# Kernel tuning notes

Measured on AMD Instinct MI355X. Metric: run time of the kernel, lower is better.

Reference implementation:

```python
import jax, jax.numpy as jnp
import numpy as np

N, S, EMB, H = 4, 2048, 512, 8
D = EMB // H  # 64


def setup_inputs() -> dict:
    key = jax.random.key(0)
    ks = jax.random.split(key, 10)
    sc = 0.02
    return {
        "x": jax.random.normal(ks[0], (N, S, EMB), dtype=jnp.float32),
        "Wq": jax.random.normal(ks[1], (D, D), dtype=jnp.float32) * sc,
        "bq": jax.random.normal(ks[2], (D,), dtype=jnp.float32) * sc,
        "Wk": jax.random.normal(ks[3], (D, D), dtype=jnp.float32) * sc,
        "bk": jax.random.normal(ks[4], (D,), dtype=jnp.float32) * sc,
        "Wv": jax.random.normal(ks[5], (D, D), dtype=jnp.float32) * sc,
        "bv": jax.random.normal(ks[6], (D,), dtype=jnp.float32) * sc,
        "E": jax.random.normal(ks[7], (1, S, D), dtype=jnp.float32),
        "Wo": jax.random.normal(ks[8], (EMB, EMB), dtype=jnp.float32) * sc,
        "bo": jax.random.normal(ks[9], (EMB,), dtype=jnp.float32) * sc,
    }


def reference(x, Wq, bq, Wk, bk, Wv, bv, E, Wo, bo):
    n, s, emb = x.shape
    h, d = H, D
    xh = x.reshape(n, s, h, d)
    # per-head Linear projections (torch Linear: y = x @ W.T + b)
    q = xh @ Wq.T + bq  # [n,s,h,d]
    k = xh @ Wk.T + bk
    v = xh @ Wv.T + bv

    # QE = queries.transpose(1,2) @ E.transpose(1,2) -> [n,h,s,s]
    QE = jnp.einsum('nqhd,sd->nhqs', q, E[0])
    # _mask_positions: zero where triu(ones(S,S),1) flipped along columns == 1
    triu1 = jnp.triu(jnp.ones((s, s), dtype=bool), 1)
    QE = jnp.where(triu1[:, ::-1], 0.0, QE)
    # _skew: pad last dim on the left, reinterpret (s, s+1) as (s+1, s), drop first row
    padded = jnp.pad(QE, ((0, 0), (0, 0), (0, 0), (1, 0)))  # [n,h,s,s+1]
    Smat = padded.reshape(n, h, s + 1, s)[:, :, 1:, :]  # [n,h,s,s]

    qk = jnp.einsum('nqhd,nkhd->nhqk', q, k)
    # faithful to source: fill where mask==0 (lower triangle incl. diag) with -1e20
    qk = jnp.where(triu1, qk, jnp.float32(-1e20))
    attention = jax.nn.softmax(qk / (emb ** 0.5), axis=3) + Smat

    z = jnp.einsum('nhql,nlhd->nqhd', attention, v).reshape(n, s, h * d)
    return z @ Wo.T + bo


if __name__ == "__main__":
    out = reference(**setup_inputs())
    print(out.shape, out.dtype)
```

## Files before the change

kernel.cpp:

```cpp
#include <hip/hip_runtime.h>
#include <hip/hip_bf16.h>

#define S_LEN 2048
#define EMB   512
#define NH    8
#define DH    64
#define NB    4

typedef float f32x4  __attribute__((ext_vector_type(4)));
typedef short short8 __attribute__((ext_vector_type(8)));

__device__ __forceinline__ unsigned short f2bf_rn(float f) {
    return __builtin_bit_cast(unsigned short, __float2bfloat16(f));
}

__device__ __forceinline__ f32x4 mfma16(short8 a, short8 b, f32x4 c) {
    return __builtin_amdgcn_mfma_f32_16x16x32_bf16(a, b, c, 0, 0, 0);
}

__device__ __forceinline__ short8 frag_read(const unsigned short* lds, int row, int oct)
{
    const char* src = (const char*)lds + row * 128 + ((oct * 16) ^ ((row & 7) << 4));
    return *reinterpret_cast<const short8*>(src);
}

__device__ __forceinline__ int pinv(int k) {
    return (k & 32) + ((k >> 2) & 3) * 8 + (k & 3) + ((k & 16) >> 2);
}

__device__ __forceinline__ void stage_tile_bf16(const unsigned short* __restrict__ g,
                                                int gstride, unsigned short* lds, int tid)
{
    #pragma unroll
    for (int c = tid; c < 512; c += 256) {
        const int r = c >> 3, s = c & 7;
        short8 v = *reinterpret_cast<const short8*>(g + (size_t)r * gstride + s * 8);
        char* dst = (char*)lds + r * 128 + ((s * 16) ^ ((r & 7) << 4));
        *reinterpret_cast<short8*>(dst) = v;
    }
}

__device__ __forceinline__ void softmax_pack(const f32x4 C[4], bool diag, int ws, int og,
                                             int rowg, float& dsum, short8& pa0, short8& pa1)
{
    constexpr float SM_SC2 = 0.06375861597263857f;
    float rs[4];
    unsigned short pw[16];
    if (!diag) {
        #pragma unroll
        for (int t = 0; t < 4; ++t) {
            float a = 0.f;
            #pragma unroll
            for (int r = 0; r < 4; ++r) {
                const float wv = __builtin_exp2f(C[t][r] * SM_SC2);
                a += wv;
                pw[t * 4 + r] = f2bf_rn(wv);
            }
            rs[t] = a;
        }
    } else {
        #pragma unroll
        for (int t = 0; t < 4; ++t) {
            float a = 0.f;
            #pragma unroll
            for (int r = 0; r < 4; ++r) {
                const bool keep = (t > ws) || (t == ws && (og * 4 + r) > rowg);
                const float wv = keep ? __builtin_exp2f(C[t][r] * SM_SC2) : 0.f;
                a += wv;
                pw[t * 4 + r] = f2bf_rn(wv);
            }
            rs[t] = a;
        }
    }
    dsum += (rs[0] + rs[1]) + (rs[2] + rs[3]);
    #pragma unroll
    for (int i = 0; i < 8; ++i) { pa0[i] = (short)pw[i]; pa1[i] = (short)pw[8 + i]; }
}

__global__ __launch_bounds__(256) void prep_w(
    const float* __restrict__ Wq, const float* __restrict__ Wk,
    const float* __restrict__ Wv, const float* __restrict__ Wo,
    unsigned short* __restrict__ wq, unsigned short* __restrict__ wk,
    unsigned short* __restrict__ wv, unsigned short* __restrict__ wo)
{
    const int i = blockIdx.x * 256 + threadIdx.x;
    if (i < 4096) {
        wq[i] = f2bf_rn(Wq[i]);
        wk[i] = f2bf_rn(Wk[i]);
        wv[i] = f2bf_rn(Wv[i]);
    }
    if (i < EMB * EMB) wo[i] = f2bf_rn(Wo[i]);
}

__global__ __launch_bounds__(256) void qkv_mfma(
    const float* __restrict__ x,
    const unsigned short* __restrict__ Wqb, const float* __restrict__ bq,
    const unsigned short* __restrict__ Wkb, const float* __restrict__ bk,
    const unsigned short* __restrict__ Wvb, const float* __restrict__ bv,
    unsigned short* __restrict__ qg, unsigned short* __restrict__ kg,
    unsigned short* __restrict__ vg)
{
    __shared__ unsigned short w_lds[3][64 * 64];

    const int tid  = threadIdx.x;
    const int lane = tid & 63;
    const int w    = tid >> 6;
    const int rowg = lane & 15;
    const int og   = lane >> 4;

    stage_tile_bf16(Wqb, 64, w_lds[0], tid);
    stage_tile_bf16(Wkb, 64, w_lds[1], tid);
    stage_tile_bf16(Wvb, 64, w_lds[2], tid);

    float bias[3][4];
    #pragma unroll
    for (int t = 0; t < 4; ++t) {
        bias[0][t] = bq[16 * t + rowg];
        bias[1][t] = bk[16 * t + rowg];
        bias[2][t] = bv[16 * t + rowg];
    }

    const int m0 = blockIdx.x * 64 + 16 * w;
    const float* xr = x + (size_t)(m0 + rowg) * 64;
    const float4 a0 = *(const float4*)(xr + og * 8);
    const float4 a1 = *(const float4*)(xr + og * 8 + 4);
    const float4 a2 = *(const float4*)(xr + 32 + og * 8);
    const float4 a3 = *(const float4*)(xr + 32 + og * 8 + 4);
    short8 af0, af1;
    af0[0] = (short)f2bf_rn(a0.x); af0[1] = (short)f2bf_rn(a0.y);
    af0[2] = (short)f2bf_rn(a0.z); af0[3] = (short)f2bf_rn(a0.w);
    af0[4] = (short)f2bf_rn(a1.x); af0[5] = (short)f2bf_rn(a1.y);
    af0[6] = (short)f2bf_rn(a1.z); af0[7] = (short)f2bf_rn(a1.w);
    af1[0] = (short)f2bf_rn(a2.x); af1[1] = (short)f2bf_rn(a2.y);
    af1[2] = (short)f2bf_rn(a2.z); af1[3] = (short)f2bf_rn(a2.w);
    af1[4] = (short)f2bf_rn(a3.x); af1[5] = (short)f2bf_rn(a3.y);
    af1[6] = (short)f2bf_rn(a3.z); af1[7] = (short)f2bf_rn(a3.w);

    __syncthreads();

    f32x4 acc[3][4];
    #pragma unroll
    for (int m = 0; m < 3; ++m)
        #pragma unroll
        for (int t = 0; t < 4; ++t) {
            const float b = bias[m][t];
            acc[m][t] = (f32x4){b, b, b, b};
        }

    #pragma unroll
    for (int m = 0; m < 3; ++m)
        #pragma unroll
        for (int t = 0; t < 4; ++t) {
            acc[m][t] = mfma16(af0, frag_read(w_lds[m], 16 * t + rowg, og),     acc[m][t]);
            acc[m][t] = mfma16(af1, frag_read(w_lds[m], 16 * t + rowg, og + 4), acc[m][t]);
        }

    unsigned short* outp[3] = {qg, kg, vg};
    #pragma unroll
    for (int m = 0; m < 3; ++m)
        #pragma unroll
        for (int r = 0; r < 4; ++r) {
            const int mr = (blockIdx.x * 64 + 16 * w) + og * 4 + r;
            const int tk = mr >> 3, h = mr & 7;
            const int n = tk >> 11, s = tk & 2047;
            const size_t rowb = (((size_t)(n * NH + h)) * S_LEN + s) * 64;
            #pragma unroll
            for (int t = 0; t < 4; ++t)
                outp[m][rowb + 16 * t + rowg] = f2bf_rn(acc[m][t][r]);
        }
}

__global__ __launch_bounds__(256) void transpose_v(
    const unsigned short* __restrict__ v, unsigned short* __restrict__ vt)
{
    __shared__ unsigned short t_lds[64][72];
    const int bid = blockIdx.x;
    const int st = bid % (S_LEN / 64);
    const int nh = bid / (S_LEN / 64);
    const unsigned short* vp = v + ((size_t)nh * S_LEN + st * 64) * DH;
    unsigned short* vtp = vt + (size_t)nh * DH * S_LEN + st * 64;
    const int tid = threadIdx.x;
    #pragma unroll
    for (int c = tid; c < 512; c += 256) {
        const int r = c >> 3, s = c & 7;
        short8 xv = *reinterpret_cast<const short8*>(vp + r * DH + s * 8);
        #pragma unroll
        for (int i = 0; i < 8; ++i) t_lds[s * 8 + i][r] = (unsigned short)xv[i];
    }
    __syncthreads();
    #pragma unroll
    for (int c = tid; c < 512; c += 256) {
        const int d = c >> 3, sc = c & 7;
        const int cb = ((sc & 4) << 3) + (sc & 3) * 4;
        short8 y;
        #pragma unroll
        for (int i = 0; i < 8; ++i)
            y[i] = (short)t_lds[d][cb + (i & 3) + ((i & 4) << 2)];
        *reinterpret_cast<short8*>(vtp + (size_t)d * S_LEN + sc * 8) = y;
    }
}

__global__ __launch_bounds__(256) void prep_e(
    const float* __restrict__ E, unsigned short* __restrict__ eb)
{
    const int i = blockIdx.x * 256 + threadIdx.x;
    if (i >= S_LEN * DH) return;
    const int dlt = i >> 6, d = i & 63;
    eb[i] = f2bf_rn(E[(size_t)(S_LEN - 1 - dlt) * DH + d]);
}

__global__ __launch_bounds__(256) void attn_mfma(
    const unsigned short* __restrict__ qg,
    const unsigned short* __restrict__ kg,
    const unsigned short* __restrict__ vtg,
    const unsigned short* __restrict__ eg,
    unsigned short* __restrict__ z)
{
    __shared__ __align__(16) unsigned short smem[20480];

    constexpr float UNI = 1.0f / 2048.0f;

    const int nqt = S_LEN / 64;
    const int bid = blockIdx.x;
    const int qt  = (nqt - 1) - (bid >> 5);
    const int nh  = bid & 31;
    const int q0  = qt * 64;
    const size_t base = (size_t)nh * S_LEN * DH;
    const unsigned short* qp = qg + base;
    const unsigned short* kp = kg + base;
    const unsigned short* vp = vtg + base;

    const int tid  = threadIdx.x;
    const int lane = tid & 63;
    const int w    = tid >> 6;
    const int rowg = lane & 15;
    const int og   = lane >> 4;

    const int r0 = tid >> 3,  s0 = tid & 7;
    const int r1 = r0 + 32;
    const int ldsoff0 = r0 * 128 + ((s0 * 16) ^ ((r0 & 7) << 4));
    const int ldsoff1 = r1 * 128 + ((s0 * 16) ^ ((r1 & 7) << 4));
    const int ksrc0 = r0 * 64 + s0 * 8,    ksrc1 = r1 * 64 + s0 * 8;
    const int vsrc0 = r0 * S_LEN + s0 * 8, vsrc1 = r1 * S_LEN + s0 * 8;

    short8 kr0, kr1, vr0, vr1;

    short8 qa0, qa1;
    {
        const unsigned short* qr = qp + (size_t)(q0 + 16 * w + rowg) * DH + og * 8;
        qa0 = *reinterpret_cast<const short8*>(qr);
        qa1 = *reinterpret_cast<const short8*>(qr + 32);
    }

    const f32x4 zero4 = {0.f, 0.f, 0.f, 0.f};
    f32x4 accS[4], accR[4];
    #pragma unroll
    for (int t = 0; t < 4; ++t) { accS[t] = zero4; accR[t] = zero4; }
    float dsum = 0.f;

    const int T = (S_LEN - q0) >> 6;
    kr0 = *(const short8*)(kp + (size_t)q0 * 64 + ksrc0);
    kr1 = *(const short8*)(kp + (size_t)q0 * 64 + ksrc1);
    vr0 = *(const short8*)(vp + q0 + vsrc0);
    vr1 = *(const short8*)(vp + q0 + vsrc1);
    *(short8*)((char*)smem + ldsoff0) = kr0;
    *(short8*)((char*)smem + ldsoff1) = kr1;
    *(short8*)((char*)(smem + 8192) + ldsoff0) = vr0;
    *(short8*)((char*)(smem + 8192) + ldsoff1) = vr1;
    __syncthreads();

    short8 pa0, pa1;
    for (int ti = 0; ti < T; ++ti) {
        const bool pf = (ti + 1 < T);
        if (pf) {
            const unsigned short* kb = kp + (size_t)(q0 + (ti + 1) * 64) * 64;
            const unsigned short* vb = vp + (q0 + (ti + 1) * 64);
            kr0 = *(const short8*)(kb + ksrc0);
            kr1 = *(const short8*)(kb + ksrc1);
            vr0 = *(const short8*)(vb + vsrc0);
            vr1 = *(const short8*)(vb + vsrc1);
        }
        const unsigned short* klds = smem + (ti & 1) * 4096;

        __builtin_amdgcn_s_setprio(1);
        f32x4 C[4];
        #pragma unroll
        for (int t = 0; t < 4; ++t) {
            const short8 kf0 = frag_read(klds, 16 * t + rowg, og);
            const short8 kf1 = frag_read(klds, 16 * t + rowg, og + 4);
            C[t] = mfma16(kf1, qa1, mfma16(kf0, qa0, zero4));
        }
        if (ti > 0) {
            const unsigned short* vprev = smem + 8192 + ((ti + 2) % 3) * 4096;
            #pragma unroll
            for (int tt = 0; tt < 4; ++tt) {
                const short8 vf0 = frag_read(vprev, 16 * tt + rowg, og);
                const short8 vf1 = frag_read(vprev, 16 * tt + rowg, og + 4);
                accS[tt] = mfma16(pa1, vf1, mfma16(pa0, vf0, accS[tt]));
            }
        }
        __builtin_amdgcn_s_setprio(0);

        if (pf) {
            unsigned short* kn = smem + ((ti + 1) & 1) * 4096;
            unsigned short* vn = smem + 8192 + ((ti + 1) % 3) * 4096;
            *(short8*)((char*)kn + ldsoff0) = kr0;
            *(short8*)((char*)kn + ldsoff1) = kr1;
            *(short8*)((char*)vn + ldsoff0) = vr0;
            *(short8*)((char*)vn + ldsoff1) = vr1;
        }
        softmax_pack(C, ti == 0, w, og, rowg, dsum, pa0, pa1);
        __syncthreads();
    }
    {
        const unsigned short* vprev = smem + 8192 + ((T + 2) % 3) * 4096;
        __builtin_amdgcn_s_setprio(1);
        #pragma unroll
        for (int tt = 0; tt < 4; ++tt) {
            const short8 vf0 = frag_read(vprev, 16 * tt + rowg, og);
            const short8 vf1 = frag_read(vprev, 16 * tt + rowg, og + 4);
            accS[tt] = mfma16(pa1, vf1, mfma16(pa0, vf0, accS[tt]));
        }
        __builtin_amdgcn_s_setprio(0);
    }
    __syncthreads();

    unsigned short* const ebuf = smem + 16384;
    const int jmax = q0 >> 6;

    kr0 = *(const short8*)(eg + ksrc0);
    kr1 = *(const short8*)(eg + ksrc1);
    vr0 = *(const short8*)(vp + q0 + vsrc0);
    vr1 = *(const short8*)(vp + q0 + vsrc1);
    {
        const short8 z8 = {0, 0, 0, 0, 0, 0, 0, 0};
        #pragma unroll
        for (int c2 = 0; c2 < 2; ++c2) {
            const int cc = lane + 64 * c2;
            const int r = 16 * w + (cc >> 3), sc = cc & 7;
            *reinterpret_cast<short8*>((char*)smem + r * 128 + sc * 16) = z8;
        }
    }
    *(short8*)((char*)ebuf + ldsoff0) = kr0;
    *(short8*)((char*)ebuf + ldsoff1) = kr1;
    *(short8*)((char*)(smem + 8192) + ldsoff0) = vr0;
    *(short8*)((char*)(smem + 8192) + ldsoff1) = vr1;
    __syncthreads();

    for (int j = 0; j <= jmax; ++j) {
        const bool pf = (j < jmax);
        if (pf) {
            const unsigned short* ebn = eg + (size_t)(j + 1) * 4096;
            const unsigned short* vbn = vp + (q0 - 64 * (j + 1));
            kr0 = *(const short8*)(ebn + ksrc0);
            kr1 = *(const short8*)(ebn + ksrc1);
            vr0 = *(const short8*)(vbn + vsrc0);
            vr1 = *(const short8*)(vbn + vsrc1);
        }
        const unsigned short* vlds = smem + 8192 + (j & 1) * 4096;

        __builtin_amdgcn_s_setprio(1);
        f32x4 G[4];
        #pragma unroll
        for (int t = 0; t < 4; ++t)
            G[t] = mfma16(qa1, frag_read(ebuf, 16 * t + rowg, og + 4),
                   mfma16(qa0, frag_read(ebuf, 16 * t + rowg, og), zero4));
        __builtin_amdgcn_s_setprio(0);

        unsigned short* pc = smem + (j & 1) * 4096;
        unsigned short* pn = smem + ((j + 1) & 1) * 4096;
        #pragma unroll
        for (int t = 0; t < 4; ++t) {
            const int c = 16 * t + rowg;
            #pragma unroll
            for (int r = 0; r < 4; ++r) {
                const int qq = 16 * w + og * 4 + r;
                float val = G[t][r];
                if (q0 + qq == S_LEN - 1) val += UNI;
                const unsigned short bv = f2bf_rn(val);
                const int swz = (qq & 7) << 4;
                if (c <= qq) {
                    const int p = pinv(qq - c);
                    *(unsigned short*)((char*)pc + qq * 128 + ((p * 2) ^ swz)) = bv;
                } else if (pf) {
                    const int p = pinv(qq - c + 64);
                    *(unsigned short*)((char*)pn + qq * 128 + ((p * 2) ^ swz)) = bv;
                }
            }
        }

        const short8 pb0 = frag_read(pc, 16 * w + rowg, og);
        const short8 pb1 = frag_read(pc, 16 * w + rowg, og + 4);
        __builtin_amdgcn_s_setprio(1);
        #pragma unroll
        for (int tt = 0; tt < 4; ++tt) {
            const short8 vf0 = frag_read(vlds, 16 * tt + rowg, og);
            const short8 vf1 = frag_read(vlds, 16 * tt + rowg, og + 4);
            accR[tt] = mfma16(pb1, vf1, mfma16(pb0, vf0, accR[tt]));
        }
        __builtin_amdgcn_s_setprio(0);

        __syncthreads();
        if (pf) {
            unsigned short* vn = smem + 8192 + ((j + 1) & 1) * 4096;
            *(short8*)((char*)ebuf + ldsoff0) = kr0;
            *(short8*)((char*)ebuf + ldsoff1) = kr1;
            *(short8*)((char*)vn + ldsoff0) = vr0;
            *(short8*)((char*)vn + ldsoff1) = vr1;
            __syncthreads();
        }
    }

    dsum += __shfl_xor(dsum, 16);
    dsum += __shfl_xor(dsum, 32);

    const int n = nh >> 3, h = nh & 7;
    const int qrow0 = q0 + 16 * w + og * 4;
    #pragma unroll
    for (int r = 0; r < 4; ++r) {
        const int qrow = qrow0 + r;
        const float dn = __shfl(dsum, og * 4 + r);
        const float inv = (qrow == S_LEN - 1) ? 0.f : 1.f / dn;
        #pragma unroll
        for (int t = 0; t < 4; ++t) {
            const float zv = accS[t][r] * inv + accR[t][r];
            z[((size_t)n * S_LEN + qrow) * EMB + h * DH + 16 * t + rowg] = f2bf_rn(zv);
        }
    }
}

__global__ __launch_bounds__(256) void outproj_mfma(
    const unsigned short* __restrict__ z,
    const unsigned short* __restrict__ Wob, const float* __restrict__ bo,
    float* __restrict__ out)
{
    __shared__ unsigned short wo_lds[2][64 * 64];

    const int tid  = threadIdx.x;
    const int lane = tid & 63;
    const int w    = tid >> 6;
    const int rowg = lane & 15;
    const int og   = lane >> 4;

    const int nob = EMB / 64;
    const int mb = blockIdx.x / nob;
    const int ob = blockIdx.x % nob;
    const int m0 = mb * 64 + 16 * w;
    const int o0 = ob * 64;

    const int r0 = tid >> 3,  s0 = tid & 7;
    const int r1 = r0 + 32;
    const int ldsoff0 = r0 * 128 + ((s0 * 16) ^ ((r0 & 7) << 4));
    const int ldsoff1 = r1 * 128 + ((s0 * 16) ^ ((r1 & 7) << 4));
    const int wsrc0 = r0 * EMB + s0 * 8, wsrc1 = r1 * EMB + s0 * 8;
    const unsigned short* wbase = Wob + (size_t)o0 * EMB;

    f32x4 acc[4];
    #pragma unroll
    for (int t = 0; t < 4; ++t) {
        const float b = bo[o0 + 16 * t + rowg];
        acc[t] = (f32x4){b, b, b, b};
    }

    short8 wr0 = *(const short8*)(wbase + wsrc0);
    short8 wr1 = *(const short8*)(wbase + wsrc1);
    *(short8*)((char*)wo_lds[0] + ldsoff0) = wr0;
    *(short8*)((char*)wo_lds[0] + ldsoff1) = wr1;
    __syncthreads();

    int cur = 0;
    for (int kt = 0; kt < 8; ++kt) {
        const bool pf = (kt < 7);
        if (pf) {
            wr0 = *(const short8*)(wbase + (kt + 1) * 64 + wsrc0);
            wr1 = *(const short8*)(wbase + (kt + 1) * 64 + wsrc1);
        }
        const unsigned short* zr = z + (size_t)(m0 + rowg) * EMB + kt * 64;
        const short8 af0 = *reinterpret_cast<const short8*>(zr + og * 8);
        const short8 af1 = *reinterpret_cast<const short8*>(zr + 32 + og * 8);
        #pragma unroll
        for (int t = 0; t < 4; ++t) {
            acc[t] = mfma16(af0, frag_read(wo_lds[cur], 16 * t + rowg, og),     acc[t]);
            acc[t] = mfma16(af1, frag_read(wo_lds[cur], 16 * t + rowg, og + 4), acc[t]);
        }
        if (pf) {
            *(short8*)((char*)wo_lds[cur ^ 1] + ldsoff0) = wr0;
            *(short8*)((char*)wo_lds[cur ^ 1] + ldsoff1) = wr1;
        }
        __syncthreads();
        cur ^= 1;
    }

    #pragma unroll
    for (int r = 0; r < 4; ++r) {
        const size_t rowb = (size_t)(m0 + og * 4 + r) * EMB + o0;
        #pragma unroll
        for (int t = 0; t < 4; ++t)
            out[rowb + 16 * t + rowg] = acc[t][r];
    }
}

extern "C" void kernel_launch(void* const* d_in, const int* in_sizes, int n_in,
                              void* d_out, int out_size, void* d_ws, size_t ws_size,
                              hipStream_t stream) {
    const float* x  = (const float*)d_in[0];
    const float* Wq = (const float*)d_in[1];
    const float* bq = (const float*)d_in[2];
    const float* Wk = (const float*)d_in[3];
    const float* bk = (const float*)d_in[4];
    const float* Wv = (const float*)d_in[5];
    const float* bv = (const float*)d_in[6];
    const float* E  = (const float*)d_in[7];
    const float* Wo = (const float*)d_in[8];
    const float* bo = (const float*)d_in[9];
    float* out = (float*)d_out;

    const size_t per = (size_t)NB * NH * S_LEN * DH;
    unsigned short* qb  = (unsigned short*)d_ws;
    unsigned short* kb  = qb  + per;
    unsigned short* vb  = kb  + per;
    unsigned short* vtb = vb  + per;
    unsigned short* eb  = vtb + per;
    unsigned short* zb  = eb + (size_t)S_LEN * DH;
    unsigned short* wqb = zb + per * 2;
    unsigned short* wkb = wqb + 4096;
    unsigned short* wvb = wkb + 4096;
    unsigned short* wob = wvb + 4096;

    prep_w<<<(EMB * EMB + 255) / 256, 256, 0, stream>>>(Wq, Wk, Wv, Wo,
                                                        wqb, wkb, wvb, wob);
    qkv_mfma<<<(NB * S_LEN * NH) / 64, 256, 0, stream>>>(x, wqb, bq, wkb, bk, wvb, bv,
                                                         qb, kb, vb);
    transpose_v<<<NB * NH * (S_LEN / 64), 256, 0, stream>>>(vb, vtb);
    prep_e<<<(S_LEN * DH + 255) / 256, 256, 0, stream>>>(E, eb);
    attn_mfma<<<NB * NH * (S_LEN / 64), 256, 0, stream>>>(qb, kb, vtb, eb, zb);
    outproj_mfma<<<(NB * S_LEN / 64) * (EMB / 64), 256, 0, stream>>>(zb, wob, bo, out);
}
```

Measured before the change: 109.4 us.

## Load E fragments directly into registers and shrink attention LDS footprint

The relative-position phase now reads E fragments straight from global memory into registers instead of staging them through an LDS buffer. This removes one LDS buffer and one barrier per iteration. The first phase's V buffer goes from triple to double buffering, which needs an extra barrier, so LDS drops from 40KB to 32KB and occupancy may rise. The separate prep_e launch is folded into the weight-conversion kernel, removing one kernel launch. The trade-off is more vector registers held for E fragments and an extra sync in the main loop.

```diff
diff --git a/kernel.cpp b/kernel.cpp
--- a/kernel.cpp
+++ b/kernel.cpp
@@ -77,11 +77,13 @@
     for (int i = 0; i < 8; ++i) { pa0[i] = (short)pw[i]; pa1[i] = (short)pw[8 + i]; }
 }
 
-__global__ __launch_bounds__(256) void prep_w(
+__global__ __launch_bounds__(256) void prep_we(
     const float* __restrict__ Wq, const float* __restrict__ Wk,
     const float* __restrict__ Wv, const float* __restrict__ Wo,
+    const float* __restrict__ E,
     unsigned short* __restrict__ wq, unsigned short* __restrict__ wk,
-    unsigned short* __restrict__ wv, unsigned short* __restrict__ wo)
+    unsigned short* __restrict__ wv, unsigned short* __restrict__ wo,
+    unsigned short* __restrict__ eb)
 {
     const int i = blockIdx.x * 256 + threadIdx.x;
     if (i < 4096) {
@@ -90,6 +92,10 @@
         wv[i] = f2bf_rn(Wv[i]);
     }
     if (i < EMB * EMB) wo[i] = f2bf_rn(Wo[i]);
+    if (i < S_LEN * DH) {
+        const int dlt = i >> 6, d = i & 63;
+        eb[i] = f2bf_rn(E[(size_t)(S_LEN - 1 - dlt) * DH + d]);
+    }
 }
 
 __global__ __launch_bounds__(256) void qkv_mfma(
@@ -200,15 +206,6 @@
     }
 }
 
-__global__ __launch_bounds__(256) void prep_e(
-    const float* __restrict__ E, unsigned short* __restrict__ eb)
-{
-    const int i = blockIdx.x * 256 + threadIdx.x;
-    if (i >= S_LEN * DH) return;
-    const int dlt = i >> 6, d = i & 63;
-    eb[i] = f2bf_rn(E[(size_t)(S_LEN - 1 - dlt) * DH + d]);
-}
-
 __global__ __launch_bounds__(256) void attn_mfma(
     const unsigned short* __restrict__ qg,
     const unsigned short* __restrict__ kg,
@@ -216,7 +213,7 @@
     const unsigned short* __restrict__ eg,
     unsigned short* __restrict__ z)
 {
-    __shared__ __align__(16) unsigned short smem[20480];
+    __shared__ __align__(16) unsigned short smem[16384];
 
     constexpr float UNI = 1.0f / 2048.0f;
 
@@ -291,7 +288,7 @@
             C[t] = mfma16(kf1, qa1, mfma16(kf0, qa0, zero4));
         }
         if (ti > 0) {
-            const unsigned short* vprev = smem + 8192 + ((ti + 2) % 3) * 4096;
+            const unsigned short* vprev = smem + 8192 + ((ti + 1) & 1) * 4096;
             #pragma unroll
             for (int tt = 0; tt < 4; ++tt) {
                 const short8 vf0 = frag_read(vprev, 16 * tt + rowg, og);
@@ -300,10 +297,11 @@
             }
         }
         __builtin_amdgcn_s_setprio(0);
+        __syncthreads();
 
         if (pf) {
             unsigned short* kn = smem + ((ti + 1) & 1) * 4096;
-            unsigned short* vn = smem + 8192 + ((ti + 1) % 3) * 4096;
+            unsigned short* vn = smem + 8192 + ((ti + 1) & 1) * 4096;
             *(short8*)((char*)kn + ldsoff0) = kr0;
             *(short8*)((char*)kn + ldsoff1) = kr1;
             *(short8*)((char*)vn + ldsoff0) = vr0;
@@ -313,7 +311,7 @@
         __syncthreads();
     }
     {
-        const unsigned short* vprev = smem + 8192 + ((T + 2) % 3) * 4096;
+        const unsigned short* vprev = smem + 8192 + ((T + 1) & 1) * 4096;
         __builtin_amdgcn_s_setprio(1);
         #pragma unroll
         for (int tt = 0; tt < 4; ++tt) {
@@ -325,13 +323,17 @@
     }
     __syncthreads();
 
-    unsigned short* const ebuf = smem + 16384;
     const int jmax = q0 >> 6;
 
-    kr0 = *(const short8*)(eg + ksrc0);
-    kr1 = *(const short8*)(eg + ksrc1);
     vr0 = *(const short8*)(vp + q0 + vsrc0);
     vr1 = *(const short8*)(vp + q0 + vsrc1);
+    short8 ef[8];
+    #pragma unroll
+    for (int t = 0; t < 4; ++t) {
+        const unsigned short* er = eg + (size_t)(16 * t + rowg) * 64;
+        ef[t * 2]     = *(const short8*)(er + og * 8);
+        ef[t * 2 + 1] = *(const short8*)(er + (og + 4) * 8);
+    }
     {
         const short8 z8 = {0, 0, 0, 0, 0, 0, 0, 0};
         #pragma unroll
@@ -341,8 +343,6 @@
             *reinterpret_cast<short8*>((char*)smem + r * 128 + sc * 16) = z8;
         }
     }
-    *(short8*)((char*)ebuf + ldsoff0) = kr0;
-    *(short8*)((char*)ebuf + ldsoff1) = kr1;
     *(short8*)((char*)(smem + 8192) + ldsoff0) = vr0;
     *(short8*)((char*)(smem + 8192) + ldsoff1) = vr1;
     __syncthreads();
@@ -350,10 +350,7 @@
     for (int j = 0; j <= jmax; ++j) {
         const bool pf = (j < jmax);
         if (pf) {
-            const unsigned short* ebn = eg + (size_t)(j + 1) * 4096;
             const unsigned short* vbn = vp + (q0 - 64 * (j + 1));
-            kr0 = *(const short8*)(ebn + ksrc0);
-            kr1 = *(const short8*)(ebn + ksrc1);
             vr0 = *(const short8*)(vbn + vsrc0);
             vr1 = *(const short8*)(vbn + vsrc1);
         }
@@ -363,9 +360,17 @@
         f32x4 G[4];
         #pragma unroll
         for (int t = 0; t < 4; ++t)
-            G[t] = mfma16(qa1, frag_read(ebuf, 16 * t + rowg, og + 4),
-                   mfma16(qa0, frag_read(ebuf, 16 * t + rowg, og), zero4));
+            G[t] = mfma16(qa1, ef[t * 2 + 1], mfma16(qa0, ef[t * 2], zero4));
         __builtin_amdgcn_s_setprio(0);
+
+        if (pf) {
+            #pragma unroll
+            for (int t = 0; t < 4; ++t) {
+                const unsigned short* er = eg + (size_t)(64 * (j + 1) + 16 * t + rowg) * 64;
+                ef[t * 2]     = *(const short8*)(er + og * 8);
+                ef[t * 2 + 1] = *(const short8*)(er + (og + 4) * 8);
+            }
+        }
 
         unsigned short* pc = smem + (j & 1) * 4096;
         unsigned short* pn = smem + ((j + 1) & 1) * 4096;
@@ -400,15 +405,12 @@
         }
         __builtin_amdgcn_s_setprio(0);
 
-        __syncthreads();
         if (pf) {
             unsigned short* vn = smem + 8192 + ((j + 1) & 1) * 4096;
-            *(short8*)((char*)ebuf + ldsoff0) = kr0;
-            *(short8*)((char*)ebuf + ldsoff1) = kr1;
             *(short8*)((char*)vn + ldsoff0) = vr0;
             *(short8*)((char*)vn + ldsoff1) = vr1;
-            __syncthreads();
-        }
+        }
+        __syncthreads();
     }
 
     dsum += __shfl_xor(dsum, 16);
@@ -527,12 +529,11 @@
     unsigned short* wvb = wkb + 4096;
     unsigned short* wob = wvb + 4096;
 
-    prep_w<<<(EMB * EMB + 255) / 256, 256, 0, stream>>>(Wq, Wk, Wv, Wo,
-                                                        wqb, wkb, wvb, wob);
+    prep_we<<<(EMB * EMB + 255) / 256, 256, 0, stream>>>(Wq, Wk, Wv, Wo, E,
+                                                         wqb, wkb, wvb, wob, eb);
     qkv_mfma<<<(NB * S_LEN * NH) / 64, 256, 0, stream>>>(x, wqb, bq, wkb, bk, wvb, bv,
                                                          qb, kb, vb);
     transpose_v<<<NB * NH * (S_LEN / 64), 256, 0, stream>>>(vb, vtb);
-    prep_e<<<(S_LEN * DH + 255) / 256, 256, 0, stream>>>(E, eb);
     attn_mfma<<<NB * NH * (S_LEN / 64), 256, 0, stream>>>(qb, kb, vtb, eb, zb);
     outproj_mfma<<<(NB * S_LEN / 64) * (EMB / 64), 256, 0, stream>>>(zb, wob, bo, out);
 }
```

Measured after the change: 158.2 us. +44.6%, slower.
